# Optimization experiments

Hardware: AMD Instinct MI355X
Metric: run time of the kernel (lower is better)

The kernel has to match this reference:

```python
import jax, jax.numpy as jnp
import numpy as np

B, S, D = 4, 4096, 256


def setup_inputs() -> dict:
    key = jax.random.key(0)
    ks = jax.random.split(key, 8)
    scale = 1.0 / np.sqrt(D)
    inp = {
        "q": jax.random.normal(ks[0], (B, S, D), jnp.float32),
        "k": jax.random.normal(ks[1], (B, S, D), jnp.float32),
        "v": jax.random.normal(ks[2], (B, S, D), jnp.float32),
        # additive mask: 1 where attention is disallowed (causal), broadcast over batch
        "mask": jnp.triu(jnp.ones((S, S), jnp.float32), k=1)[None, :, :],
        "Wq": jax.random.normal(ks[3], (D, D), jnp.float32) * scale,
        "bq": jnp.zeros((D,), jnp.float32),
        "Wk": jax.random.normal(ks[4], (D, D), jnp.float32) * scale,
        "bk": jnp.zeros((D,), jnp.float32),
        "Wv": jax.random.normal(ks[5], (D, D), jnp.float32) * scale,
        "bv": jnp.zeros((D,), jnp.float32),
        "Wo": jax.random.normal(ks[6], (D, D), jnp.float32) * scale,
        "bo": jnp.zeros((D,), jnp.float32),
    }
    return inp


def reference(q, k, v, mask, Wq, bq, Wk, bk, Wv, bv, Wo, bo):
    # Dense projections (Keras Dense: x @ W + b)
    qp = q @ Wq + bq  # [B,S,D]
    kp = k @ Wk + bk
    vp = v @ Wv + bv
    dk = jnp.asarray(qp.shape[-1], qp.dtype)
    # scaled dot-product attention, materialized scores as in the source
    logits = jnp.einsum("bqd,bkd->bqk", qp, kp) / jnp.sqrt(dk)  # [B,S,S]
    logits = logits + mask * (-1e9)
    attn = jax.nn.softmax(logits, axis=-1)  # [B,S,S]
    ctx = jnp.einsum("bqk,bkd->bqd", attn, vp)  # [B,S,D]
    z = ctx @ Wo + bo
    return z, attn
```

## Files before the change

kernel.cpp:

```cpp
#include <hip/hip_runtime.h>


typedef unsigned short u16;
typedef __attribute__((ext_vector_type(8))) short short8;
typedef __attribute__((ext_vector_type(4))) float f32x4;

struct __align__(8) us4 { u16 x, y, z, w; };

#define SEQ 4096
#define DIM 256

__device__ __forceinline__ u16 f2bf(float f) {
  unsigned int u = __float_as_uint(f);
  u += 0x7fffu + ((u >> 16) & 1u);
  return (u16)(u >> 16);
}

__device__ __forceinline__ void cp16(const void* g, void* l) {
  __builtin_amdgcn_global_load_lds((const __attribute__((address_space(1))) void*)g,
                                   (__attribute__((address_space(3))) void*)l, 16, 0, 0);
}

__global__ void k_convert(const float* __restrict__ q, const float* __restrict__ k,
                          const float* __restrict__ v, u16* __restrict__ qb,
                          u16* __restrict__ kb, u16* __restrict__ vb) {
  const float* src = blockIdx.z == 0 ? q : (blockIdx.z == 1 ? k : v);
  u16* dst = blockIdx.z == 0 ? qb : (blockIdx.z == 1 ? kb : vb);
  size_t i4 = (size_t)blockIdx.x * 256 + threadIdx.x;
  float4 val = ((const float4*)src)[i4];
  us4 o;
  o.x = f2bf(val.x); o.y = f2bf(val.y); o.z = f2bf(val.z); o.w = f2bf(val.w);
  ((us4*)dst)[i4] = o;
}

__global__ void k_wt(const float* __restrict__ Wq, const float* __restrict__ Wk,
                     const float* __restrict__ Wv, const float* __restrict__ Wo,
                     u16* __restrict__ wt) {
  __shared__ float t[32][33];
  const float* W = blockIdx.z == 0 ? Wq : blockIdx.z == 1 ? Wk : blockIdx.z == 2 ? Wv : Wo;
  u16* out = wt + (size_t)blockIdx.z * 65536;
  int n0 = blockIdx.x * 32, k0 = blockIdx.y * 32;
  int tx = threadIdx.x, ty = threadIdx.y;
  for (int i = 0; i < 4; i++)
    t[ty + i * 8][tx] = W[(size_t)(k0 + ty + i * 8) * 256 + n0 + tx];
  __syncthreads();
  for (int i = 0; i < 4; i++)
    out[(size_t)(n0 + ty + i * 8) * 256 + k0 + tx] = f2bf(t[tx][ty + i * 8]);
}

__global__ void k_vt(const u16* __restrict__ vp, u16* __restrict__ vpt) {
  __shared__ u16 t[32][33];
  int b = blockIdx.z;
  int n0 = blockIdx.x * 32, k0 = blockIdx.y * 32;
  int tx = threadIdx.x, ty = threadIdx.y;
  const u16* src = vp + ((size_t)b << 20);
  u16* dst = vpt + ((size_t)b << 20);
  for (int i = 0; i < 4; i++)
    t[ty + i * 8][tx] = src[(size_t)(k0 + ty + i * 8) * 256 + n0 + tx];
  __syncthreads();
  for (int i = 0; i < 4; i++)
    dst[(size_t)(n0 + ty + i * 8) * 4096 + k0 + tx] = t[tx][ty + i * 8];
}

template <bool OUT_BF16>
__global__ void k_gemm(const u16* __restrict__ A, const u16* __restrict__ Wt,
                       const float* __restrict__ bias, void* __restrict__ outp) {
  __shared__ u16 Asm[128 * 32];
  __shared__ u16 Bsm[128 * 32];
  const int tid = threadIdx.x;
  const int lane = tid & 63, w = tid >> 6;
  const int wr = w >> 1, wc = w & 1;
  const int quad = lane >> 4, m16 = lane & 15;
  const int m0 = blockIdx.y * 128, n0 = blockIdx.x * 128;

  f32x4 zero = {0.f, 0.f, 0.f, 0.f};
  f32x4 acc[4][4];
  for (int i = 0; i < 4; i++)
    for (int j = 0; j < 4; j++) acc[i][j] = zero;

  for (int kk = 0; kk < 8; ++kk) {
    const int k0 = kk * 32;
    for (int h = 0; h < 2; ++h) {
      int c = tid + h * 256;
      int row = c >> 2, sub = c & 3;
      cp16(A + (size_t)(m0 + row) * 256 + k0 + sub * 8, Asm + c * 8);
      cp16(Wt + (size_t)(n0 + row) * 256 + k0 + sub * 8, Bsm + c * 8);
    }
    __syncthreads();
    short8 a[4], b[4];
    for (int i = 0; i < 4; ++i)
      a[i] = *(const short8*)(Asm + (wr * 64 + i * 16 + m16) * 32 + quad * 8);
    for (int j = 0; j < 4; ++j)
      b[j] = *(const short8*)(Bsm + (wc * 64 + j * 16 + m16) * 32 + quad * 8);
    for (int i = 0; i < 4; ++i)
      for (int j = 0; j < 4; ++j)
        acc[i][j] = __builtin_amdgcn_mfma_f32_16x16x32_bf16(a[i], b[j], acc[i][j], 0, 0, 0);
    __syncthreads();
  }

  for (int j = 0; j < 4; ++j) {
    int gn = n0 + wc * 64 + j * 16 + m16;
    float bv = bias[gn];
    for (int i = 0; i < 4; ++i) {
      int gm = m0 + wr * 64 + i * 16 + quad * 4;
      for (int r = 0; r < 4; ++r) {
        float val = acc[i][j][r] + bv;
        if (OUT_BF16)
          ((u16*)outp)[(size_t)(gm + r) * 256 + gn] = f2bf(val);
        else
          ((float*)outp)[(size_t)(gm + r) * 256 + gn] = val;
      }
    }
  }
}

__global__ void k_qk(const u16* __restrict__ qp, const u16* __restrict__ kp,
                     float* __restrict__ attn, float* __restrict__ ps) {
  const int kt = blockIdx.x, qt = blockIdx.y, bz = blockIdx.z;
  const int tid = threadIdx.x;
  const int q0 = qt * 128, k0t = kt * 128;
  float* attnb = attn + ((size_t)bz << 24);

  if (kt > qt) {
    float4 z4 = make_float4(0.f, 0.f, 0.f, 0.f);
    for (int s = 0; s < 16; ++s) {
      int idx = tid + s * 256;
      int row = idx >> 5, c4 = idx & 31;
      *(float4*)(attnb + (size_t)(q0 + row) * 4096 + k0t + c4 * 4) = z4;
    }
    if (tid < 128) ps[(size_t)(bz * 32 + kt) * 4096 + q0 + tid] = 0.f;
    return;
  }

  __shared__ __align__(16) char smem[128 * 132 * 4];
  u16* Asm = (u16*)smem;
  u16* Bsm = Asm + 128 * 32;
  float* epi = (float*)smem;
  __shared__ float prow[2][128];

  const int lane = tid & 63, w = tid >> 6;
  const int wr = w >> 1, wc = w & 1;
  const int quad = lane >> 4, m16 = lane & 15;
  const u16* Ab = qp + ((size_t)bz << 20);
  const u16* Bb = kp + ((size_t)bz << 20);

  f32x4 zero = {0.f, 0.f, 0.f, 0.f};
  f32x4 acc[4][4];
  for (int i = 0; i < 4; i++)
    for (int j = 0; j < 4; j++) acc[i][j] = zero;

  for (int kk = 0; kk < 8; ++kk) {
    const int k0 = kk * 32;
    for (int h = 0; h < 2; ++h) {
      int c = tid + h * 256;
      int row = c >> 2, sub = c & 3;
      cp16(Ab + (size_t)(q0 + row) * 256 + k0 + sub * 8, Asm + c * 8);
      cp16(Bb + (size_t)(k0t + row) * 256 + k0 + sub * 8, Bsm + c * 8);
    }
    __syncthreads();
    short8 a[4], b[4];
    for (int i = 0; i < 4; ++i)
      a[i] = *(const short8*)(Asm + (wr * 64 + i * 16 + m16) * 32 + quad * 8);
    for (int j = 0; j < 4; ++j)
      b[j] = *(const short8*)(Bsm + (wc * 64 + j * 16 + m16) * 32 + quad * 8);
    for (int i = 0; i < 4; ++i)
      for (int j = 0; j < 4; ++j)
        acc[i][j] = __builtin_amdgcn_mfma_f32_16x16x32_bf16(a[i], b[j], acc[i][j], 0, 0, 0);
    __syncthreads();
  }

  float rs[4][4];
  for (int i = 0; i < 4; i++)
    for (int r = 0; r < 4; r++) rs[i][r] = 0.f;
  for (int i = 0; i < 4; ++i) {
    int gq = q0 + wr * 64 + i * 16 + quad * 4;
    for (int j = 0; j < 4; ++j) {
      int gk = k0t + wc * 64 + j * 16 + m16;
      for (int r = 0; r < 4; ++r) {
        float e = (gk <= gq + r) ? __expf(acc[i][j][r] * 0.0625f) : 0.f;
        acc[i][j][r] = e;
        rs[i][r] += e;
      }
    }
  }
  for (int off = 1; off < 16; off <<= 1)
    for (int i = 0; i < 4; ++i)
      for (int r = 0; r < 4; ++r) rs[i][r] += __shfl_xor(rs[i][r], off, 64);
  if (m16 == 0)
    for (int i = 0; i < 4; ++i)
      for (int r = 0; r < 4; ++r)
        prow[wc][wr * 64 + i * 16 + quad * 4 + r] = rs[i][r];

  for (int i = 0; i < 4; ++i)
    for (int j = 0; j < 4; ++j) {
      int rl = (wr * 64 + i * 16 + quad * 4) * 132 + wc * 64 + j * 16 + m16;
      for (int r = 0; r < 4; ++r) epi[rl + r * 132] = acc[i][j][r];
    }
  __syncthreads();

  for (int it = 0; it < 16; ++it) {
    int idx = it * 256 + tid;
    int row = idx >> 5, c4 = idx & 31;
    float4 v4 = *(const float4*)(epi + row * 132 + c4 * 4);
    *(float4*)(attnb + (size_t)(q0 + row) * 4096 + k0t + c4 * 4) = v4;
  }
  if (tid < 128)
    ps[(size_t)(bz * 32 + kt) * 4096 + q0 + tid] = prow[0][tid] + prow[1][tid];
}

__global__ void k_rsum(const float* __restrict__ ps, float* __restrict__ inv) {
  int b = blockIdx.y;
  int q = blockIdx.x * 256 + threadIdx.x;
  float s = 0.f;
  for (int kt = 0; kt < 32; ++kt) s += ps[(size_t)(b * 32 + kt) * 4096 + q];
  inv[b * 4096 + q] = 1.f / s;
}

__global__ void k_zero(float4* __restrict__ p) {
  p[(size_t)blockIdx.x * 256 + threadIdx.x] = make_float4(0.f, 0.f, 0.f, 0.f);
}

__global__ void __launch_bounds__(512) k_pvg(float* __restrict__ attn,
                                             const u16* __restrict__ vpt,
                                             const float* __restrict__ inv,
                                             float* __restrict__ ctxf) {
  const int kg = blockIdx.x, qt = blockIdx.y, bz = blockIdx.z;
  const int k_lo = kg * 1024;
  const int k_hi = min((qt + 1) * 128, k_lo + 1024);
  if (k_lo >= k_hi) return;

  __shared__ u16 P_lds[128 * 136];
  __shared__ u16 B_lds[2][256 * 32];
  __shared__ float inv_lds[128];

  const int tid = threadIdx.x;
  const int lane = tid & 63, w = tid >> 6;
  const int wr = w >> 2, wc = w & 3;
  const int quad = lane >> 4, m16 = lane & 15;
  const int q0 = qt * 128;
  float* attnb = attn + ((size_t)bz << 24);
  const u16* vb = vpt + ((size_t)bz << 20);

  if (tid < 128) inv_lds[tid] = inv[bz * 4096 + q0 + tid];
  __syncthreads();

  f32x4 zero = {0.f, 0.f, 0.f, 0.f};
  f32x4 acc[4][4];
  for (int i = 0; i < 4; i++)
    for (int j = 0; j < 4; j++) acc[i][j] = zero;

  for (int kt0 = k_lo; kt0 < k_hi; kt0 += 128) {
    for (int p = 0; p < 8; ++p) {
      int idx = p * 512 + tid;
      int row = idx >> 5, c4 = idx & 31;
      float4* gp = (float4*)(attnb + (size_t)(q0 + row) * 4096 + kt0 + c4 * 4);
      float4 e = *gp;
      float ivr = inv_lds[row];
      e.x *= ivr; e.y *= ivr; e.z *= ivr; e.w *= ivr;
      *gp = e;
      us4 pk;
      pk.x = f2bf(e.x); pk.y = f2bf(e.y); pk.z = f2bf(e.z); pk.w = f2bf(e.w);
      *(us4*)(P_lds + row * 136 + c4 * 4) = pk;
    }
    for (int half = 0; half < 2; ++half) {
      if (half == 1) __syncthreads();
      for (int h = 0; h < 4; ++h) {
        int c = h * 512 + tid;
        int sbuf = c >> 10;
        int cc = c & 1023;
        int n = cc >> 2, sub = cc & 3;
        cp16(vb + (size_t)n * 4096 + kt0 + half * 64 + sbuf * 32 + sub * 8,
             B_lds[sbuf] + n * 32 + sub * 8);
      }
      __syncthreads();
      for (int s = 0; s < 2; ++s) {
        int klocal = half * 64 + s * 32;
        short8 a[4], b[4];
        for (int i = 0; i < 4; ++i)
          a[i] = *(const short8*)(P_lds + (wr * 64 + i * 16 + m16) * 136 + klocal + quad * 8);
        for (int j = 0; j < 4; ++j)
          b[j] = *(const short8*)(B_lds[s] + (wc * 64 + j * 16 + m16) * 32 + quad * 8);
        for (int i = 0; i < 4; ++i)
          for (int j = 0; j < 4; ++j)
            acc[i][j] = __builtin_amdgcn_mfma_f32_16x16x32_bf16(a[i], b[j], acc[i][j], 0, 0, 0);
      }
    }
    __syncthreads();
  }

  for (int i = 0; i < 4; ++i) {
    int gq = q0 + wr * 64 + i * 16 + quad * 4;
    for (int j = 0; j < 4; ++j) {
      int gn = wc * 64 + j * 16 + m16;
      for (int r = 0; r < 4; ++r)
        atomicAdd(&ctxf[((size_t)bz * 4096 + gq + r) * 256 + gn], acc[i][j][r]);
    }
  }
}

__global__ void k_cvt(const float* __restrict__ ctxf, u16* __restrict__ ctx) {
  size_t i4 = (size_t)blockIdx.x * 256 + threadIdx.x;
  float4 v = ((const float4*)ctxf)[i4];
  us4 o;
  o.x = f2bf(v.x); o.y = f2bf(v.y); o.z = f2bf(v.z); o.w = f2bf(v.w);
  ((us4*)ctx)[i4] = o;
}

extern "C" void kernel_launch(void* const* d_in, const int* in_sizes, int n_in,
                              void* d_out, int out_size, void* d_ws, size_t ws_size,
                              hipStream_t stream) {
  const float* q  = (const float*)d_in[0];
  const float* k  = (const float*)d_in[1];
  const float* v  = (const float*)d_in[2];
  const float* Wq = (const float*)d_in[4];
  const float* bq = (const float*)d_in[5];
  const float* Wk = (const float*)d_in[6];
  const float* bk = (const float*)d_in[7];
  const float* Wv = (const float*)d_in[8];
  const float* bv = (const float*)d_in[9];
  const float* Wo = (const float*)d_in[10];
  const float* bo = (const float*)d_in[11];

  const size_t MD = (size_t)16384 * 256;
  u16* qb = (u16*)d_ws;
  u16* kb = qb + MD;
  u16* vb = kb + MD;
  u16* qp = vb + MD;
  u16* kp = qp + MD;
  u16* vp = kp + MD;
  u16* wt = vp + MD;
  float* ps   = (float*)(wt + 4 * 65536);
  float* inv  = ps + (size_t)4 * 32 * 4096;
  float* ctxf = inv + (size_t)4 * 4096;
  u16* vpt = kb;
  u16* ctx = qb;

  float* zout = (float*)d_out;
  float* attn = zout + (size_t)4 * 4096 * 256;

  k_convert<<<dim3(4096, 1, 3), 256, 0, stream>>>(q, k, v, qb, kb, vb);
  k_wt<<<dim3(8, 8, 4), dim3(32, 8), 0, stream>>>(Wq, Wk, Wv, Wo, wt);
  k_gemm<true><<<dim3(2, 128), 256, 0, stream>>>(qb, wt, bq, qp);
  k_gemm<true><<<dim3(2, 128), 256, 0, stream>>>(kb, wt + 65536, bk, kp);
  k_gemm<true><<<dim3(2, 128), 256, 0, stream>>>(vb, wt + 2 * 65536, bv, vp);
  k_vt<<<dim3(8, 128, 4), dim3(32, 8), 0, stream>>>(vp, vpt);
  k_qk<<<dim3(32, 32, 4), 256, 0, stream>>>(qp, kp, attn, ps);
  k_rsum<<<dim3(16, 4), 256, 0, stream>>>(ps, inv);
  k_zero<<<4096, 256, 0, stream>>>((float4*)ctxf);
  k_pvg<<<dim3(4, 32, 4), 512, 0, stream>>>(attn, vpt, inv, ctxf);
  k_cvt<<<4096, 256, 0, stream>>>(ctxf, ctx);
  k_gemm<false><<<dim3(2, 128), 256, 0, stream>>>(ctx, wt + 3 * 65536, bo, zout);
}
```

Before: 595.4 us.

## Fuse input conversion and V transpose into projection GEMMs; stage scores as bf16

Projection GEMMs now read fp32 inputs and convert them to bf16 while loading, which removes the separate conversion kernel. The V projection writes its output already transposed, which removes the transpose kernel. The QK kernel writes unnormalized exponentials to a bf16 scratch buffer instead of fp32 attn, and the PV kernel reads that buffer and writes the normalized attn once. This cuts the fp32 read-modify-write traffic on the large score matrix, and nontemporal stores and loads are added. The trade-off is that attn now carries bf16 rounding of the probabilities, and an extra workspace buffer is needed.

```diff
diff --git a/kernel.cpp b/kernel.cpp
--- a/kernel.cpp
+++ b/kernel.cpp
@@ -4,6 +4,7 @@
 typedef unsigned short u16;
 typedef __attribute__((ext_vector_type(8))) short short8;
 typedef __attribute__((ext_vector_type(4))) float f32x4;
+typedef __attribute__((ext_vector_type(4))) unsigned short u16x4;
 
 struct __align__(8) us4 { u16 x, y, z, w; };
 
@@ -15,22 +16,13 @@
   u += 0x7fffu + ((u >> 16) & 1u);
   return (u16)(u >> 16);
 }
+__device__ __forceinline__ float bf2f(u16 u) {
+  return __uint_as_float(((unsigned int)u) << 16);
+}
 
 __device__ __forceinline__ void cp16(const void* g, void* l) {
   __builtin_amdgcn_global_load_lds((const __attribute__((address_space(1))) void*)g,
                                    (__attribute__((address_space(3))) void*)l, 16, 0, 0);
-}
-
-__global__ void k_convert(const float* __restrict__ q, const float* __restrict__ k,
-                          const float* __restrict__ v, u16* __restrict__ qb,
-                          u16* __restrict__ kb, u16* __restrict__ vb) {
-  const float* src = blockIdx.z == 0 ? q : (blockIdx.z == 1 ? k : v);
-  u16* dst = blockIdx.z == 0 ? qb : (blockIdx.z == 1 ? kb : vb);
-  size_t i4 = (size_t)blockIdx.x * 256 + threadIdx.x;
-  float4 val = ((const float4*)src)[i4];
-  us4 o;
-  o.x = f2bf(val.x); o.y = f2bf(val.y); o.z = f2bf(val.z); o.w = f2bf(val.w);
-  ((us4*)dst)[i4] = o;
 }
 
 __global__ void k_wt(const float* __restrict__ Wq, const float* __restrict__ Wk,
@@ -48,18 +40,286 @@
     out[(size_t)(n0 + ty + i * 8) * 256 + k0 + tx] = f2bf(t[tx][ty + i * 8]);
 }
 
-__global__ void k_vt(const u16* __restrict__ vp, u16* __restrict__ vpt) {
-  __shared__ u16 t[32][33];
-  int b = blockIdx.z;
-  int n0 = blockIdx.x * 32, k0 = blockIdx.y * 32;
-  int tx = threadIdx.x, ty = threadIdx.y;
-  const u16* src = vp + ((size_t)b << 20);
-  u16* dst = vpt + ((size_t)b << 20);
-  for (int i = 0; i < 4; i++)
-    t[ty + i * 8][tx] = src[(size_t)(k0 + ty + i * 8) * 256 + n0 + tx];
+template <bool TRANS>
+__global__ void k_pgemm(const float* __restrict__ A, const u16* __restrict__ Wt,
+                        const float* __restrict__ bias, u16* __restrict__ outp) {
+  __shared__ __align__(16) char smem[34816];
+  u16* Asm = (u16*)smem;
+  u16* Bsm = Asm + 4096;
+  u16* tb = (u16*)smem;
+  const int tid = threadIdx.x;
+  const int lane = tid & 63, w = tid >> 6;
+  const int wr = w >> 1, wc = w & 1;
+  const int quad = lane >> 4, m16 = lane & 15;
+  const int m0 = blockIdx.y * 128, n0 = blockIdx.x * 128;
+
+  f32x4 zero = {0.f, 0.f, 0.f, 0.f};
+  f32x4 acc[4][4];
+  for (int i = 0; i < 4; i++)
+    for (int j = 0; j < 4; j++) acc[i][j] = zero;
+
+  for (int kk = 0; kk < 8; ++kk) {
+    const int k0 = kk * 32;
+    for (int h = 0; h < 2; ++h) {
+      int c = tid + h * 256;
+      int row = c >> 2, sub = c & 3;
+      cp16(Wt + (size_t)(n0 + row) * 256 + k0 + sub * 8, Bsm + c * 8);
+    }
+    for (int h = 0; h < 4; ++h) {
+      int idx = h * 256 + tid;
+      int row = idx >> 3, q4 = idx & 7;
+      float4 a4 = *(const float4*)(A + (size_t)(m0 + row) * 256 + k0 + q4 * 4);
+      us4 o;
+      o.x = f2bf(a4.x); o.y = f2bf(a4.y); o.z = f2bf(a4.z); o.w = f2bf(a4.w);
+      *(us4*)(Asm + row * 32 + q4 * 4) = o;
+    }
+    __syncthreads();
+    short8 a[4], b[4];
+    for (int i = 0; i < 4; ++i)
+      a[i] = *(const short8*)(Asm + (wr * 64 + i * 16 + m16) * 32 + quad * 8);
+    for (int j = 0; j < 4; ++j)
+      b[j] = *(const short8*)(Bsm + (wc * 64 + j * 16 + m16) * 32 + quad * 8);
+    for (int i = 0; i < 4; ++i)
+      for (int j = 0; j < 4; ++j)
+        acc[i][j] = __builtin_amdgcn_mfma_f32_16x16x32_bf16(a[i], b[j], acc[i][j], 0, 0, 0);
+    __syncthreads();
+  }
+
+  if (!TRANS) {
+    for (int j = 0; j < 4; ++j) {
+      int gn = n0 + wc * 64 + j * 16 + m16;
+      float bv = bias[gn];
+      for (int i = 0; i < 4; ++i) {
+        int gm = m0 + wr * 64 + i * 16 + quad * 4;
+        for (int r = 0; r < 4; ++r)
+          outp[(size_t)(gm + r) * 256 + gn] = f2bf(acc[i][j][r] + bv);
+      }
+    }
+  } else {
+    for (int j = 0; j < 4; ++j) {
+      int cn = wc * 64 + j * 16 + m16;
+      float bv = bias[n0 + cn];
+      for (int i = 0; i < 4; ++i) {
+        int rm = wr * 64 + i * 16 + quad * 4;
+        us4 o;
+        o.x = f2bf(acc[i][j][0] + bv); o.y = f2bf(acc[i][j][1] + bv);
+        o.z = f2bf(acc[i][j][2] + bv); o.w = f2bf(acc[i][j][3] + bv);
+        *(us4*)(tb + cn * 136 + rm) = o;
+      }
+    }
+    __syncthreads();
+    int b = m0 >> 12, s0 = m0 & 4095;
+    u16* dst = outp + ((size_t)b << 20);
+    for (int it = 0; it < 8; ++it) {
+      int idx = it * 256 + tid;
+      int n = idx >> 4, m8 = idx & 15;
+      short8 v8 = *(const short8*)(tb + n * 136 + m8 * 8);
+      *(short8*)(dst + (size_t)(n0 + n) * 4096 + s0 + m8 * 8) = v8;
+    }
+  }
+}
+
+__global__ void k_qk(const u16* __restrict__ qp, const u16* __restrict__ kp,
+                     u16* __restrict__ eb, float* __restrict__ attn,
+                     float* __restrict__ ps) {
+  const int kt = blockIdx.x, qt = blockIdx.y, bz = blockIdx.z;
+  const int tid = threadIdx.x;
+  const int q0 = qt * 128, k0t = kt * 128;
+
+  if (kt > qt) {
+    float* attnb = attn + ((size_t)bz << 24);
+    f32x4 z4 = {0.f, 0.f, 0.f, 0.f};
+    for (int s = 0; s < 16; ++s) {
+      int idx = tid + s * 256;
+      int row = idx >> 5, c4 = idx & 31;
+      __builtin_nontemporal_store(z4,
+          (f32x4*)(attnb + (size_t)(q0 + row) * 4096 + k0t + c4 * 4));
+    }
+    if (tid < 128) ps[(size_t)(bz * 32 + kt) * 4096 + q0 + tid] = 0.f;
+    return;
+  }
+
+  __shared__ __align__(16) char smem[34816];
+  u16* Asm = (u16*)smem;
+  u16* Bsm = Asm + 4096;
+  u16* epi = (u16*)smem;
+  __shared__ float prow[2][128];
+
+  const int lane = tid & 63, w = tid >> 6;
+  const int wr = w >> 1, wc = w & 1;
+  const int quad = lane >> 4, m16 = lane & 15;
+  const u16* Ab = qp + ((size_t)bz << 20);
+  const u16* Bb = kp + ((size_t)bz << 20);
+
+  f32x4 zero = {0.f, 0.f, 0.f, 0.f};
+  f32x4 acc[4][4];
+  for (int i = 0; i < 4; i++)
+    for (int j = 0; j < 4; j++) acc[i][j] = zero;
+
+  for (int kk = 0; kk < 8; ++kk) {
+    const int k0 = kk * 32;
+    for (int h = 0; h < 2; ++h) {
+      int c = tid + h * 256;
+      int row = c >> 2, sub = c & 3;
+      cp16(Ab + (size_t)(q0 + row) * 256 + k0 + sub * 8, Asm + c * 8);
+      cp16(Bb + (size_t)(k0t + row) * 256 + k0 + sub * 8, Bsm + c * 8);
+    }
+    __syncthreads();
+    short8 a[4], b[4];
+    for (int i = 0; i < 4; ++i)
+      a[i] = *(const short8*)(Asm + (wr * 64 + i * 16 + m16) * 32 + quad * 8);
+    for (int j = 0; j < 4; ++j)
+      b[j] = *(const short8*)(Bsm + (wc * 64 + j * 16 + m16) * 32 + quad * 8);
+    for (int i = 0; i < 4; ++i)
+      for (int j = 0; j < 4; ++j)
+        acc[i][j] = __builtin_amdgcn_mfma_f32_16x16x32_bf16(a[i], b[j], acc[i][j], 0, 0, 0);
+    __syncthreads();
+  }
+
+  float rs[4][4];
+  for (int i = 0; i < 4; i++)
+    for (int r = 0; r < 4; r++) rs[i][r] = 0.f;
+  for (int i = 0; i < 4; ++i) {
+    int gq = q0 + wr * 64 + i * 16 + quad * 4;
+    for (int j = 0; j < 4; ++j) {
+      int gk = k0t + wc * 64 + j * 16 + m16;
+      for (int r = 0; r < 4; ++r) {
+        float e = (gk <= gq + r) ? __expf(acc[i][j][r] * 0.0625f) : 0.f;
+        acc[i][j][r] = e;
+        rs[i][r] += e;
+      }
+    }
+  }
+  for (int off = 1; off < 16; off <<= 1)
+    for (int i = 0; i < 4; ++i)
+      for (int r = 0; r < 4; ++r) rs[i][r] += __shfl_xor(rs[i][r], off, 64);
+  if (m16 == 0)
+    for (int i = 0; i < 4; ++i)
+      for (int r = 0; r < 4; ++r)
+        prow[wc][wr * 64 + i * 16 + quad * 4 + r] = rs[i][r];
+
+  for (int i = 0; i < 4; ++i)
+    for (int j = 0; j < 4; ++j) {
+      int rl = wr * 64 + i * 16 + quad * 4;
+      int cl = wc * 64 + j * 16 + m16;
+      for (int r = 0; r < 4; ++r) epi[(rl + r) * 136 + cl] = f2bf(acc[i][j][r]);
+    }
   __syncthreads();
-  for (int i = 0; i < 4; i++)
-    dst[(size_t)(n0 + ty + i * 8) * 4096 + k0 + tx] = t[tx][ty + i * 8];
+
+  u16* ebb = eb + ((size_t)bz << 24);
+  for (int it = 0; it < 8; ++it) {
+    int idx = it * 256 + tid;
+    int row = idx >> 4, m8 = idx & 15;
+    short8 v8 = *(const short8*)(epi + row * 136 + m8 * 8);
+    __builtin_nontemporal_store(v8,
+        (short8*)(ebb + (size_t)(q0 + row) * 4096 + k0t + m8 * 8));
+  }
+  if (tid < 128)
+    ps[(size_t)(bz * 32 + kt) * 4096 + q0 + tid] = prow[0][tid] + prow[1][tid];
+}
+
+__global__ void k_rsum(const float* __restrict__ ps, float* __restrict__ inv) {
+  int b = blockIdx.y;
+  int q = blockIdx.x * 256 + threadIdx.x;
+  float s = 0.f;
+  for (int kt = 0; kt < 32; ++kt) s += ps[(size_t)(b * 32 + kt) * 4096 + q];
+  inv[b * 4096 + q] = 1.f / s;
+}
+
+__global__ void k_zero(float4* __restrict__ p) {
+  p[(size_t)blockIdx.x * 256 + threadIdx.x] = make_float4(0.f, 0.f, 0.f, 0.f);
+}
+
+__global__ void __launch_bounds__(512) k_pv2(const u16* __restrict__ eb,
+                                             const u16* __restrict__ vpt,
+                                             const float* __restrict__ inv,
+                                             float* __restrict__ attn,
+                                             float* __restrict__ ctxf) {
+  const int kg = blockIdx.x, qt = blockIdx.y, bz = blockIdx.z;
+  const int k_lo = kg * 1024;
+  const int k_hi = min((qt + 1) * 128, k_lo + 1024);
+  if (k_lo >= k_hi) return;
+
+  __shared__ u16 P_lds[128 * 136];
+  __shared__ u16 B_lds[2][256 * 32];
+  __shared__ float inv_lds[128];
+
+  const int tid = threadIdx.x;
+  const int lane = tid & 63, w = tid >> 6;
+  const int wr = w >> 2, wc = w & 3;
+  const int quad = lane >> 4, m16 = lane & 15;
+  const int q0 = qt * 128;
+  const u16* ebb = eb + ((size_t)bz << 24);
+  float* attnb = attn + ((size_t)bz << 24);
+  const u16* vb = vpt + ((size_t)bz << 20);
+
+  if (tid < 128) inv_lds[tid] = inv[bz * 4096 + q0 + tid];
+  __syncthreads();
+
+  f32x4 zero = {0.f, 0.f, 0.f, 0.f};
+  f32x4 acc[4][4];
+  for (int i = 0; i < 4; i++)
+    for (int j = 0; j < 4; j++) acc[i][j] = zero;
+
+  for (int kt0 = k_lo; kt0 < k_hi; kt0 += 128) {
+    for (int p = 0; p < 8; ++p) {
+      int idx = p * 512 + tid;
+      int row = idx >> 5, c4 = idx & 31;
+      u16x4 e4 = __builtin_nontemporal_load(
+          (const u16x4*)(ebb + (size_t)(q0 + row) * 4096 + kt0 + c4 * 4));
+      float ivr = inv_lds[row];
+      f32x4 pv;
+      us4 pk;
+      pk.x = f2bf(bf2f(e4[0]) * ivr); pv[0] = bf2f(pk.x);
+      pk.y = f2bf(bf2f(e4[1]) * ivr); pv[1] = bf2f(pk.y);
+      pk.z = f2bf(bf2f(e4[2]) * ivr); pv[2] = bf2f(pk.z);
+      pk.w = f2bf(bf2f(e4[3]) * ivr); pv[3] = bf2f(pk.w);
+      *(us4*)(P_lds + row * 136 + c4 * 4) = pk;
+      __builtin_nontemporal_store(pv,
+          (f32x4*)(attnb + (size_t)(q0 + row) * 4096 + kt0 + c4 * 4));
+    }
+    for (int half = 0; half < 2; ++half) {
+      if (half == 1) __syncthreads();
+      for (int h = 0; h < 4; ++h) {
+        int c = h * 512 + tid;
+        int sbuf = c >> 10;
+        int cc = c & 1023;
+        int n = cc >> 2, sub = cc & 3;
+        cp16(vb + (size_t)n * 4096 + kt0 + half * 64 + sbuf * 32 + sub * 8,
+             B_lds[sbuf] + n * 32 + sub * 8);
+      }
+      __syncthreads();
+      for (int s = 0; s < 2; ++s) {
+        int klocal = half * 64 + s * 32;
+        short8 a[4], b[4];
+        for (int i = 0; i < 4; ++i)
+          a[i] = *(const short8*)(P_lds + (wr * 64 + i * 16 + m16) * 136 + klocal + quad * 8);
+        for (int j = 0; j < 4; ++j)
+          b[j] = *(const short8*)(B_lds[s] + (wc * 64 + j * 16 + m16) * 32 + quad * 8);
+        for (int i = 0; i < 4; ++i)
+          for (int j = 0; j < 4; ++j)
+            acc[i][j] = __builtin_amdgcn_mfma_f32_16x16x32_bf16(a[i], b[j], acc[i][j], 0, 0, 0);
+      }
+    }
+    __syncthreads();
+  }
+
+  for (int i = 0; i < 4; ++i) {
+    int gq = q0 + wr * 64 + i * 16 + quad * 4;
+    for (int j = 0; j < 4; ++j) {
+      int gn = wc * 64 + j * 16 + m16;
+      for (int r = 0; r < 4; ++r)
+        atomicAdd(&ctxf[((size_t)bz * 4096 + gq + r) * 256 + gn], acc[i][j][r]);
+    }
+  }
+}
+
+__global__ void k_cvt(const float* __restrict__ ctxf, u16* __restrict__ ctx) {
+  size_t i4 = (size_t)blockIdx.x * 256 + threadIdx.x;
+  float4 v = ((const float4*)ctxf)[i4];
+  us4 o;
+  o.x = f2bf(v.x); o.y = f2bf(v.y); o.z = f2bf(v.z); o.w = f2bf(v.w);
+  ((us4*)ctx)[i4] = o;
 }
 
 template <bool OUT_BF16>
@@ -112,198 +372,6 @@
       }
     }
   }
-}
-
-__global__ void k_qk(const u16* __restrict__ qp, const u16* __restrict__ kp,
-                     float* __restrict__ attn, float* __restrict__ ps) {
-  const int kt = blockIdx.x, qt = blockIdx.y, bz = blockIdx.z;
-  const int tid = threadIdx.x;
-  const int q0 = qt * 128, k0t = kt * 128;
-  float* attnb = attn + ((size_t)bz << 24);
-
-  if (kt > qt) {
-    float4 z4 = make_float4(0.f, 0.f, 0.f, 0.f);
-    for (int s = 0; s < 16; ++s) {
-      int idx = tid + s * 256;
-      int row = idx >> 5, c4 = idx & 31;
-      *(float4*)(attnb + (size_t)(q0 + row) * 4096 + k0t + c4 * 4) = z4;
-    }
-    if (tid < 128) ps[(size_t)(bz * 32 + kt) * 4096 + q0 + tid] = 0.f;
-    return;
-  }
-
-  __shared__ __align__(16) char smem[128 * 132 * 4];
-  u16* Asm = (u16*)smem;
-  u16* Bsm = Asm + 128 * 32;
-  float* epi = (float*)smem;
-  __shared__ float prow[2][128];
-
-  const int lane = tid & 63, w = tid >> 6;
-  const int wr = w >> 1, wc = w & 1;
-  const int quad = lane >> 4, m16 = lane & 15;
-  const u16* Ab = qp + ((size_t)bz << 20);
-  const u16* Bb = kp + ((size_t)bz << 20);
-
-  f32x4 zero = {0.f, 0.f, 0.f, 0.f};
-  f32x4 acc[4][4];
-  for (int i = 0; i < 4; i++)
-    for (int j = 0; j < 4; j++) acc[i][j] = zero;
-
-  for (int kk = 0; kk < 8; ++kk) {
-    const int k0 = kk * 32;
-    for (int h = 0; h < 2; ++h) {
-      int c = tid + h * 256;
-      int row = c >> 2, sub = c & 3;
-      cp16(Ab + (size_t)(q0 + row) * 256 + k0 + sub * 8, Asm + c * 8);
-      cp16(Bb + (size_t)(k0t + row) * 256 + k0 + sub * 8, Bsm + c * 8);
-    }
-    __syncthreads();
-    short8 a[4], b[4];
-    for (int i = 0; i < 4; ++i)
-      a[i] = *(const short8*)(Asm + (wr * 64 + i * 16 + m16) * 32 + quad * 8);
-    for (int j = 0; j < 4; ++j)
-      b[j] = *(const short8*)(Bsm + (wc * 64 + j * 16 + m16) * 32 + quad * 8);
-    for (int i = 0; i < 4; ++i)
-      for (int j = 0; j < 4; ++j)
-        acc[i][j] = __builtin_amdgcn_mfma_f32_16x16x32_bf16(a[i], b[j], acc[i][j], 0, 0, 0);
-    __syncthreads();
-  }
-
-  float rs[4][4];
-  for (int i = 0; i < 4; i++)
-    for (int r = 0; r < 4; r++) rs[i][r] = 0.f;
-  for (int i = 0; i < 4; ++i) {
-    int gq = q0 + wr * 64 + i * 16 + quad * 4;
-    for (int j = 0; j < 4; ++j) {
-      int gk = k0t + wc * 64 + j * 16 + m16;
-      for (int r = 0; r < 4; ++r) {
-        float e = (gk <= gq + r) ? __expf(acc[i][j][r] * 0.0625f) : 0.f;
-        acc[i][j][r] = e;
-        rs[i][r] += e;
-      }
-    }
-  }
-  for (int off = 1; off < 16; off <<= 1)
-    for (int i = 0; i < 4; ++i)
-      for (int r = 0; r < 4; ++r) rs[i][r] += __shfl_xor(rs[i][r], off, 64);
-  if (m16 == 0)
-    for (int i = 0; i < 4; ++i)
-      for (int r = 0; r < 4; ++r)
-        prow[wc][wr * 64 + i * 16 + quad * 4 + r] = rs[i][r];
-
-  for (int i = 0; i < 4; ++i)
-    for (int j = 0; j < 4; ++j) {
-      int rl = (wr * 64 + i * 16 + quad * 4) * 132 + wc * 64 + j * 16 + m16;
-      for (int r = 0; r < 4; ++r) epi[rl + r * 132] = acc[i][j][r];
-    }
-  __syncthreads();
-
-  for (int it = 0; it < 16; ++it) {
-    int idx = it * 256 + tid;
-    int row = idx >> 5, c4 = idx & 31;
-    float4 v4 = *(const float4*)(epi + row * 132 + c4 * 4);
-    *(float4*)(attnb + (size_t)(q0 + row) * 4096 + k0t + c4 * 4) = v4;
-  }
-  if (tid < 128)
-    ps[(size_t)(bz * 32 + kt) * 4096 + q0 + tid] = prow[0][tid] + prow[1][tid];
-}
-
-__global__ void k_rsum(const float* __restrict__ ps, float* __restrict__ inv) {
-  int b = blockIdx.y;
-  int q = blockIdx.x * 256 + threadIdx.x;
-  float s = 0.f;
-  for (int kt = 0; kt < 32; ++kt) s += ps[(size_t)(b * 32 + kt) * 4096 + q];
-  inv[b * 4096 + q] = 1.f / s;
-}
-
-__global__ void k_zero(float4* __restrict__ p) {
-  p[(size_t)blockIdx.x * 256 + threadIdx.x] = make_float4(0.f, 0.f, 0.f, 0.f);
-}
-
-__global__ void __launch_bounds__(512) k_pvg(float* __restrict__ attn,
-                                             const u16* __restrict__ vpt,
-                                             const float* __restrict__ inv,
-                                             float* __restrict__ ctxf) {
-  const int kg = blockIdx.x, qt = blockIdx.y, bz = blockIdx.z;
-  const int k_lo = kg * 1024;
-  const int k_hi = min((qt + 1) * 128, k_lo + 1024);
-  if (k_lo >= k_hi) return;
-
-  __shared__ u16 P_lds[128 * 136];
-  __shared__ u16 B_lds[2][256 * 32];
-  __shared__ float inv_lds[128];
-
-  const int tid = threadIdx.x;
-  const int lane = tid & 63, w = tid >> 6;
-  const int wr = w >> 2, wc = w & 3;
-  const int quad = lane >> 4, m16 = lane & 15;
-  const int q0 = qt * 128;
-  float* attnb = attn + ((size_t)bz << 24);
-  const u16* vb = vpt + ((size_t)bz << 20);
-
-  if (tid < 128) inv_lds[tid] = inv[bz * 4096 + q0 + tid];
-  __syncthreads();
-
-  f32x4 zero = {0.f, 0.f, 0.f, 0.f};
-  f32x4 acc[4][4];
-  for (int i = 0; i < 4; i++)
-    for (int j = 0; j < 4; j++) acc[i][j] = zero;
-
-  for (int kt0 = k_lo; kt0 < k_hi; kt0 += 128) {
-    for (int p = 0; p < 8; ++p) {
-      int idx = p * 512 + tid;
-      int row = idx >> 5, c4 = idx & 31;
-      float4* gp = (float4*)(attnb + (size_t)(q0 + row) * 4096 + kt0 + c4 * 4);
-      float4 e = *gp;
-      float ivr = inv_lds[row];
-      e.x *= ivr; e.y *= ivr; e.z *= ivr; e.w *= ivr;
-      *gp = e;
-      us4 pk;
-      pk.x = f2bf(e.x); pk.y = f2bf(e.y); pk.z = f2bf(e.z); pk.w = f2bf(e.w);
-      *(us4*)(P_lds + row * 136 + c4 * 4) = pk;
-    }
-    for (int half = 0; half < 2; ++half) {
-      if (half == 1) __syncthreads();
-      for (int h = 0; h < 4; ++h) {
-        int c = h * 512 + tid;
-        int sbuf = c >> 10;
-        int cc = c & 1023;
-        int n = cc >> 2, sub = cc & 3;
-        cp16(vb + (size_t)n * 4096 + kt0 + half * 64 + sbuf * 32 + sub * 8,
-             B_lds[sbuf] + n * 32 + sub * 8);
-      }
-      __syncthreads();
-      for (int s = 0; s < 2; ++s) {
-        int klocal = half * 64 + s * 32;
-        short8 a[4], b[4];
-        for (int i = 0; i < 4; ++i)
-          a[i] = *(const short8*)(P_lds + (wr * 64 + i * 16 + m16) * 136 + klocal + quad * 8);
-        for (int j = 0; j < 4; ++j)
-          b[j] = *(const short8*)(B_lds[s] + (wc * 64 + j * 16 + m16) * 32 + quad * 8);
-        for (int i = 0; i < 4; ++i)
-          for (int j = 0; j < 4; ++j)
-            acc[i][j] = __builtin_amdgcn_mfma_f32_16x16x32_bf16(a[i], b[j], acc[i][j], 0, 0, 0);
-      }
-    }
-    __syncthreads();
-  }
-
-  for (int i = 0; i < 4; ++i) {
-    int gq = q0 + wr * 64 + i * 16 + quad * 4;
-    for (int j = 0; j < 4; ++j) {
-      int gn = wc * 64 + j * 16 + m16;
-      for (int r = 0; r < 4; ++r)
-        atomicAdd(&ctxf[((size_t)bz * 4096 + gq + r) * 256 + gn], acc[i][j][r]);
-    }
-  }
-}
-
-__global__ void k_cvt(const float* __restrict__ ctxf, u16* __restrict__ ctx) {
-  size_t i4 = (size_t)blockIdx.x * 256 + threadIdx.x;
-  float4 v = ((const float4*)ctxf)[i4];
-  us4 o;
-  o.x = f2bf(v.x); o.y = f2bf(v.y); o.z = f2bf(v.z); o.w = f2bf(v.w);
-  ((us4*)ctx)[i4] = o;
 }
 
 extern "C" void kernel_launch(void* const* d_in, const int* in_sizes, int n_in,
@@ -322,32 +390,27 @@
   const float* bo = (const float*)d_in[11];
 
   const size_t MD = (size_t)16384 * 256;
-  u16* qb = (u16*)d_ws;
-  u16* kb = qb + MD;
-  u16* vb = kb + MD;
-  u16* qp = vb + MD;
-  u16* kp = qp + MD;
-  u16* vp = kp + MD;
-  u16* wt = vp + MD;
+  u16* qp  = (u16*)d_ws;
+  u16* kp  = qp + MD;
+  u16* vpt = kp + MD;
+  u16* ctx = vpt + MD;
+  u16* wt  = ctx + MD;
   float* ps   = (float*)(wt + 4 * 65536);
   float* inv  = ps + (size_t)4 * 32 * 4096;
   float* ctxf = inv + (size_t)4 * 4096;
-  u16* vpt = kb;
-  u16* ctx = qb;
+  u16* eb = (u16*)(ctxf + MD);
 
   float* zout = (float*)d_out;
   float* attn = zout + (size_t)4 * 4096 * 256;
 
-  k_convert<<<dim3(4096, 1, 3), 256, 0, stream>>>(q, k, v, qb, kb, vb);
   k_wt<<<dim3(8, 8, 4), dim3(32, 8), 0, stream>>>(Wq, Wk, Wv, Wo, wt);
-  k_gemm<true><<<dim3(2, 128), 256, 0, stream>>>(qb, wt, bq, qp);
-  k_gemm<true><<<dim3(2, 128), 256, 0, stream>>>(kb, wt + 65536, bk, kp);
-  k_gemm<true><<<dim3(2, 128), 256, 0, stream>>>(vb, wt + 2 * 65536, bv, vp);
-  k_vt<<<dim3(8, 128, 4), dim3(32, 8), 0, stream>>>(vp, vpt);
-  k_qk<<<dim3(32, 32, 4), 256, 0, stream>>>(qp, kp, attn, ps);
+  k_pgemm<false><<<dim3(2, 128), 256, 0, stream>>>(q, wt, bq, qp);
+  k_pgemm<false><<<dim3(2, 128), 256, 0, stream>>>(k, wt + 65536, bk, kp);
+  k_pgemm<true><<<dim3(2, 128), 256, 0, stream>>>(v, wt + 2 * 65536, bv, vpt);
+  k_qk<<<dim3(32, 32, 4), 256, 0, stream>>>(qp, kp, eb, attn, ps);
   k_rsum<<<dim3(16, 4), 256, 0, stream>>>(ps, inv);
   k_zero<<<4096, 256, 0, stream>>>((float4*)ctxf);
-  k_pvg<<<dim3(4, 32, 4), 512, 0, stream>>>(attn, vpt, inv, ctxf);
+  k_pv2<<<dim3(4, 32, 4), 512, 0, stream>>>(eb, vpt, inv, attn, ctxf);
   k_cvt<<<4096, 256, 0, stream>>>(ctxf, ctx);
   k_gemm<false><<<dim3(2, 128), 256, 0, stream>>>(ctx, wt + 3 * 65536, bo, zout);
 }
```

New measurement: 580.3 us. -2.5%, faster.
